# Kernel tuning notes

Hardware: AMD Instinct MI355X
Metric: run time of the kernel (lower is better)

The kernel has to match this reference:

```python
import jax, jax.numpy as jnp
import numpy as np

N = 50000        # nodes
E = 1600000      # edges (avg degree 32)
F = 256          # feature_dim
H = 128          # hidden_dim
ED = 32          # edge_dim
C = 2            # num_classes
GAMMA, ZETA = -0.1, 1.1   # hard-concrete stretch bounds


def setup_inputs() -> dict:
    key = jax.random.key(0)
    ks = jax.random.split(key, 16)
    def p(i, shape, fan):
        return jax.random.normal(ks[i], shape, dtype=jnp.float32) * np.float32(1.0 / np.sqrt(fan))
    return {
        "x": jax.random.normal(ks[0], (N, F), dtype=jnp.float32),
        "edge_index": jax.random.randint(ks[1], (2, E), 0, N, dtype=jnp.int64),
        # edge scorer: Linear(2F -> ED) split into src/dst halves, then Linear(ED -> 1)
        "we_src": p(2, (F, ED), 2 * F),
        "we_dst": p(3, (F, ED), 2 * F),
        "be": jnp.zeros((ED,), jnp.float32),
        "we2": p(4, (ED,), ED),
        "be2": jnp.zeros((), jnp.float32),
        # node transform conv: Linear(F -> H)
        "wc": p(5, (F, H), F),
        "bc": jnp.zeros((H,), jnp.float32),
        # classifier: Linear(H -> H//2), LayerNorm(H//2), spectral_norm(Linear(H//2 -> C))
        "w1": p(6, (H, H // 2), H),
        "b1": jnp.zeros((H // 2,), jnp.float32),
        "ln_g": jnp.ones((H // 2,), jnp.float32),
        "ln_b": jnp.zeros((H // 2,), jnp.float32),
        "w2": p(7, (H // 2, C), H // 2),
        "b2": jnp.zeros((C,), jnp.float32),
    }


def reference(x, edge_index, we_src, we_dst, be, we2, be2, wc, bc,
              w1, b1, ln_g, ln_b, w2, b2):
    src, dst = edge_index[0], edge_index[1]
    n = x.shape[0]

    # --- edge scoring: MLP on (x_src, x_dst); project per-node first, then gather ---
    ps = x @ we_src                       # [N, ED]
    pd = x @ we_dst                       # [N, ED]
    e_h = jax.nn.relu(ps[src] + pd[dst] + be)   # [E, ED]
    logit = e_h @ we2 + be2               # [E]

    # --- hard-concrete L0 gate (deterministic / eval form) ---
    s = jax.nn.sigmoid(logit)
    gate = jnp.clip(s * (ZETA - GAMMA) + GAMMA, 0.0, 1.0)   # [E]

    # --- node transform + edge-gated message passing ---
    h = jax.nn.relu(x @ wc + bc)                            # [N, H]
    agg = jax.ops.segment_sum(gate[:, None] * h[src], dst, num_segments=n)  # [N, H]
    deg = jax.ops.segment_sum(gate, dst, num_segments=n)                    # [N]
    h_out = h + agg / (deg[:, None] + 1e-6)

    # --- edge-weighted attention pooling: attend by gated degree ---
    att = jax.nn.softmax(deg)             # [N]
    g = att @ h_out                       # [H]

    # --- classifier: Linear -> ReLU -> LayerNorm -> spectral_norm(Linear) ---
    z = jax.nn.relu(g @ w1 + b1)          # [H//2]
    mn = z.mean()
    v = ((z - mn) ** 2).mean()
    zn = (z - mn) / jnp.sqrt(v + 1e-5) * ln_g + ln_b
    sigma = jnp.linalg.norm(w2, ord=2)    # spectral norm of weight
    logits = zn @ (w2 / sigma) + b2       # [C]
    return logits
```

## Files before the change

kernel.cpp:

```cpp
#include <hip/hip_runtime.h>
#include <hip/hip_bf16.h>
#include <math.h>

constexpr int F  = 256;
constexpr int ED = 32;
constexpr int H  = 128;
constexpr int NB = 64;
constexpr int SLICE_MAX = 6272;
constexpr int CAP = 26624;
constexpr float CSH = 60.0f;

typedef __attribute__((ext_vector_type(8))) short    short8v;
typedef __attribute__((ext_vector_type(4))) float    float4v;
typedef __attribute__((ext_vector_type(8))) _Float16 half8v;

static __device__ __forceinline__ unsigned short f2bf(float f) {
    unsigned int u = __float_as_uint(f);
    unsigned int r = (u + 0x7FFFu + ((u >> 16) & 1u)) >> 16;
    return (unsigned short)r;
}

__global__ __launch_bounds__(256) void pack_kernel(
    const float* __restrict__ we_src, const float* __restrict__ we_dst,
    const float* __restrict__ wc, unsigned short* __restrict__ Wp,
    float* __restrict__ zbase, int zcount)
{
    if (blockIdx.x >= 24) {
        int zi = (blockIdx.x - 24) * 256 + threadIdx.x;
        if (zi < zcount) zbase[zi] = 0.0f;
        return;
    }
    int id = blockIdx.x * 256 + threadIdx.x;
    if (id >= 12 * 8 * 64) return;
    int lane = id & 63;
    int ks   = (id >> 6) & 7;
    int tile = id >> 9;
    int col  = tile * 16 + (lane & 15);
    int kb   = ks * 32 + (lane >> 4) * 8;

    short8v v;
    #pragma unroll
    for (int j = 0; j < 8; ++j) {
        int k = kb + j;
        float w;
        if (col < 32)       w = we_src[k * ED + col];
        else if (col < 64)  w = we_dst[k * ED + (col - 32)];
        else                w = wc[k * H + (col - 64)];
        v[j] = (short)f2bf(w);
    }
    *(short8v*)(Wp + (size_t)id * 8) = v;
}

__global__ __launch_bounds__(1024) void scatter_kernel(
    const int* __restrict__ ei, int* __restrict__ cursor,
    unsigned* __restrict__ sd, int E, int SL)
{
    __shared__ int lh[NB];
    __shared__ int lbase[NB];
    const int t = threadIdx.x;
    if (t < NB) lh[t] = 0;
    __syncthreads();

    const int e0 = blockIdx.x * 2048 + t;
    unsigned c0 = 0, c1 = 0;
    int k0 = 0, r0 = 0, k1 = 0, r1 = 0;
    const bool v0 = (e0 < E);
    const bool v1 = (e0 + 1024 < E);
    if (v0) {
        int s = ei[e0], d = ei[E + e0];
        int i = (int)((unsigned)s / (unsigned)SL);
        int j = (int)((unsigned)d / (unsigned)SL);
        k0 = i * 8 + j;
        c0 = (unsigned)(s - i * SL) | ((unsigned)(d - j * SL) << 16);
        r0 = atomicAdd(&lh[k0], 1);
    }
    if (v1) {
        int s = ei[e0 + 1024], d = ei[E + e0 + 1024];
        int i = (int)((unsigned)s / (unsigned)SL);
        int j = (int)((unsigned)d / (unsigned)SL);
        k1 = i * 8 + j;
        c1 = (unsigned)(s - i * SL) | ((unsigned)(d - j * SL) << 16);
        r1 = atomicAdd(&lh[k1], 1);
    }
    __syncthreads();
    if (t < NB && lh[t] > 0) lbase[t] = atomicAdd(&cursor[t], lh[t]);
    __syncthreads();
    if (v0) {
        int idx = lbase[k0] + r0;
        if (idx < CAP) sd[(size_t)k0 * CAP + idx] = c0;
    }
    if (v1) {
        int idx = lbase[k1] + r1;
        if (idx < CAP) sd[(size_t)k1 * CAP + idx] = c1;
    }
}

__global__ __launch_bounds__(256) void gemm_kernel(
    const float* __restrict__ x, const unsigned short* __restrict__ Wp,
    const float* __restrict__ bc,
    _Float16* __restrict__ psh, _Float16* __restrict__ pdh,
    _Float16* __restrict__ hh, int M16)
{
    __shared__ __align__(16) unsigned char As[16 * 512];

    const int t    = threadIdx.x;
    const int w    = t >> 6;
    const int lane = t & 63;

    const short8v* WpV = (const short8v*)Wp;
    short8v Bfr[3][8];
    #pragma unroll
    for (int ct = 0; ct < 3; ++ct)
        #pragma unroll
        for (int ks = 0; ks < 8; ++ks)
            Bfr[ct][ks] = WpV[(((w * 3 + ct) * 8 + ks) << 6) + lane];

    const int srow = t >> 4;
    const int sseg = t & 15;
    const int ssw  = (srow & 7) << 4;

    const int arow = lane & 15;
    const int asw  = (arow & 7) << 4;
    const int akb  = (lane >> 4) * 16;

    const int crow0 = (lane >> 4) * 4;
    const int ccol  = lane & 15;

    for (int rt = blockIdx.x; rt < M16; rt += gridDim.x) {
        const int n0 = rt * 16;
        {
            const float4* src = (const float4*)(x + (size_t)(n0 + srow) * F + sseg * 16);
            float4 f0 = src[0], f1 = src[1], f2 = src[2], f3 = src[3];
            short8v lo, hi;
            lo[0] = (short)f2bf(f0.x); lo[1] = (short)f2bf(f0.y);
            lo[2] = (short)f2bf(f0.z); lo[3] = (short)f2bf(f0.w);
            lo[4] = (short)f2bf(f1.x); lo[5] = (short)f2bf(f1.y);
            lo[6] = (short)f2bf(f1.z); lo[7] = (short)f2bf(f1.w);
            hi[0] = (short)f2bf(f2.x); hi[1] = (short)f2bf(f2.y);
            hi[2] = (short)f2bf(f2.z); hi[3] = (short)f2bf(f2.w);
            hi[4] = (short)f2bf(f3.x); hi[5] = (short)f2bf(f3.y);
            hi[6] = (short)f2bf(f3.z); hi[7] = (short)f2bf(f3.w);
            *(short8v*)&As[srow * 512 + ((sseg * 32 +  0) ^ ssw)] = lo;
            *(short8v*)&As[srow * 512 + ((sseg * 32 + 16) ^ ssw)] = hi;
        }
        __syncthreads();

        float4v accs[3];
        #pragma unroll
        for (int ct = 0; ct < 3; ++ct) accs[ct] = (float4v){0.f, 0.f, 0.f, 0.f};

        #pragma unroll
        for (int ks = 0; ks < 8; ++ks) {
            short8v a = *(const short8v*)&As[arow * 512 + ((ks * 64 + akb) ^ asw)];
            accs[0] = __builtin_amdgcn_mfma_f32_16x16x32_bf16(a, Bfr[0][ks], accs[0], 0, 0, 0);
            accs[1] = __builtin_amdgcn_mfma_f32_16x16x32_bf16(a, Bfr[1][ks], accs[1], 0, 0, 0);
            accs[2] = __builtin_amdgcn_mfma_f32_16x16x32_bf16(a, Bfr[2][ks], accs[2], 0, 0, 0);
        }

        #pragma unroll
        for (int ct = 0; ct < 3; ++ct) {
            const int gcol = w * 48 + ct * 16 + ccol;
            #pragma unroll
            for (int r = 0; r < 4; ++r) {
                const int row = n0 + crow0 + r;
                float v = accs[ct][r];
                if (gcol < 32) {
                    psh[(size_t)row * ED + gcol] = (_Float16)v;
                } else if (gcol < 64) {
                    pdh[(size_t)row * ED + (gcol - 32)] = (_Float16)v;
                } else {
                    float b = bc[gcol - 64];
                    hh[(size_t)row * H + (gcol - 64)] = (_Float16)fmaxf(v + b, 0.f);
                }
            }
        }
        __syncthreads();
    }
}

__global__ __launch_bounds__(1024) void edge_gate_kernel(
    const unsigned* __restrict__ sd, const int* __restrict__ cnt,
    const _Float16* __restrict__ psh, const _Float16* __restrict__ pdh,
    const float* __restrict__ be, const float* __restrict__ we2,
    const float* __restrict__ be2,
    _Float16* __restrict__ gateh, float* __restrict__ deg, int N, int SL)
{
    __shared__ float sbe[ED], swe2[ED];
    __shared__ float sdeg[SLICE_MAX];
    const int t = threadIdx.x;
    if (t < ED) { sbe[t] = be[t]; swe2[t] = we2[t]; }
    for (int idx = t; idx < SLICE_MAX; idx += 1024) sdeg[idx] = 0.0f;
    __syncthreads();

    const int j = blockIdx.x & 7;
    const int k = blockIdx.x >> 3;
    const int i = k >> 3;
    const int p = k & 7;
    const int bucket = i * 8 + j;
    const int start = bucket * CAP;
    const int len   = min(cnt[bucket], CAP);
    const int cs = start + (len * p) / 8;
    const int ce = start + (len * (p + 1)) / 8;
    const int ibase = i * SL;
    const int jbase = j * SL;
    const int jlen  = min(SL, N - jbase);
    const int seg = t & 3;

    for (int base = cs; base < ce; base += 256) {
        const int e = base + (t >> 2);
        if (e < ce) {
            const unsigned code = sd[e];
            const int sl = (int)(code & 0xFFFFu);
            const int dl = (int)(code >> 16);
            half8v a  = *(const half8v*)(psh + (size_t)(ibase + sl) * ED + seg * 8);
            half8v bb = *(const half8v*)(pdh + (size_t)(jbase + dl) * ED + seg * 8);
            float part = 0.f;
            #pragma unroll
            for (int jj = 0; jj < 8; ++jj) {
                int kk = seg * 8 + jj;
                part += fmaxf((float)a[jj] + (float)bb[jj] + sbe[kk], 0.f) * swe2[kk];
            }
            part += __shfl_xor(part, 1);
            part += __shfl_xor(part, 2);
            if (seg == 0) {
                float logit = part + be2[0];
                float sg = 1.0f / (1.0f + expf(-logit));
                float gt = fminf(fmaxf(sg * 1.2f - 0.1f, 0.0f), 1.0f);
                gateh[e] = (_Float16)gt;
                if (gt > 0.0f) atomicAdd(&sdeg[dl], gt);
            }
        }
    }
    __syncthreads();

    float* dst = deg + jbase;
    for (int idx = t; idx < jlen; idx += 1024) {
        float v = sdeg[idx];
        if (v != 0.0f) atomicAdd(&dst[idx], v);
    }
}

__global__ __launch_bounds__(1024) void edge_u_kernel(
    const unsigned* __restrict__ sd, const int* __restrict__ cnt,
    const _Float16* __restrict__ gateh, const float* __restrict__ deg,
    float* __restrict__ uraw, int N, int SL)
{
    __shared__ float su[SLICE_MAX];
    const int t = threadIdx.x;
    for (int idx = t; idx < SLICE_MAX; idx += 1024) su[idx] = 0.0f;
    __syncthreads();

    const int j = blockIdx.x & 7;
    const int k = blockIdx.x >> 3;
    const int i = k >> 3;
    const int p = k & 7;
    const int bucket = i * 8 + j;
    const int start = bucket * CAP;
    const int len   = min(cnt[bucket], CAP);
    const int cs = start + (len * p) / 8;
    const int ce = start + (len * (p + 1)) / 8;
    const int ibase = i * SL;
    const int jbase = j * SL;
    const int ilen  = min(SL, N - ibase);

    for (int e = cs + t; e < ce; e += 1024) {
        float gt = (float)gateh[e];
        if (gt != 0.f) {
            unsigned code = sd[e];
            int sl = (int)(code & 0xFFFFu);
            int dl = (int)(code >> 16);
            float dg = deg[jbase + dl];
            float cv = expf(dg - CSH) / (dg + 1e-6f);
            atomicAdd(&su[sl], gt * cv);
        }
    }
    __syncthreads();

    float* dst = uraw + ibase;
    for (int idx = t; idx < ilen; idx += 1024) {
        float v = su[idx];
        if (v != 0.0f) atomicAdd(&dst[idx], v);
    }
}

__global__ __launch_bounds__(256) void pool_kernel(
    const _Float16* __restrict__ hh, const float* __restrict__ deg,
    const float* __restrict__ uraw,
    float* __restrict__ gacc, float* __restrict__ S, int N)
{
    __shared__ float red[16][128];
    const int t = threadIdx.x;
    const int lane = t & 15;
    const int row  = t >> 4;

    float acc[8];
    #pragma unroll
    for (int q = 0; q < 8; ++q) acc[q] = 0.f;
    float sexp = 0.f;

    for (int n = blockIdx.x * 16 + row; n < N; n += gridDim.x * 16) {
        float ex  = expf(deg[n] - CSH);
        float wgt = ex + uraw[n];
        half8v hv = *(const half8v*)(hh + (size_t)n * H + lane * 8);
        #pragma unroll
        for (int q = 0; q < 8; ++q) acc[q] += wgt * (float)hv[q];
        if (lane == 0) sexp += ex;
    }
    sexp += __shfl_xor(sexp, 16);
    sexp += __shfl_xor(sexp, 32);
    if ((t & 63) == 0 && sexp != 0.f) atomicAdd(S, sexp);

    #pragma unroll
    for (int q = 0; q < 8; ++q) red[row][lane * 8 + q] = acc[q];
    __syncthreads();
    if (t < 128) {
        float s = 0.f;
        #pragma unroll
        for (int r = 0; r < 16; ++r) s += red[r][t];
        if (s != 0.f) atomicAdd(&gacc[t], s);
    }
}

__global__ __launch_bounds__(64) void cls_kernel(
    const float* __restrict__ gacc, const float* __restrict__ S,
    const float* __restrict__ w1, const float* __restrict__ b1,
    const float* __restrict__ ln_g, const float* __restrict__ ln_b,
    const float* __restrict__ w2, const float* __restrict__ b2,
    float* __restrict__ out)
{
    __shared__ float gs[H];
    const int t = threadIdx.x;
    const float invS = 1.0f / S[0];
    gs[t]      = gacc[t]      * invS;
    gs[t + 64] = gacc[t + 64] * invS;
    __syncthreads();

    float acc = b1[t];
    #pragma unroll 4
    for (int k = 0; k < H; ++k) acc += gs[k] * w1[k * 64 + t];
    float z = fmaxf(acc, 0.f);

    float sm = z;
    #pragma unroll
    for (int m = 1; m < 64; m <<= 1) sm += __shfl_xor(sm, m);
    float mn = sm * (1.0f / 64.0f);
    float dv = (z - mn) * (z - mn);
    float sv = dv;
    #pragma unroll
    for (int m = 1; m < 64; m <<= 1) sv += __shfl_xor(sv, m);
    float var = sv * (1.0f / 64.0f);

    float zn = (z - mn) * rsqrtf(var + 1e-5f) * ln_g[t] + ln_b[t];

    float w20 = w2[t * 2 + 0];
    float w21 = w2[t * 2 + 1];
    float ga = w20 * w20, gb = w20 * w21, gc = w21 * w21;
    float p0 = zn * w20, p1 = zn * w21;
    #pragma unroll
    for (int m = 1; m < 64; m <<= 1) {
        ga += __shfl_xor(ga, m);
        gb += __shfl_xor(gb, m);
        gc += __shfl_xor(gc, m);
        p0 += __shfl_xor(p0, m);
        p1 += __shfl_xor(p1, m);
    }
    if (t == 0) {
        float tr = ga + gc;
        float df = ga - gc;
        float eig = 0.5f * (tr + sqrtf(df * df + 4.0f * gb * gb));
        float sigma = sqrtf(eig);
        out[0] = p0 / sigma + b2[0];
        out[1] = p1 / sigma + b2[1];
    }
}

extern "C" void kernel_launch(void* const* d_in, const int* in_sizes, int n_in,
                              void* d_out, int out_size, void* d_ws, size_t ws_size,
                              hipStream_t stream) {
    const float* x      = (const float*)d_in[0];
    const int*   ei     = (const int*)  d_in[1];
    const float* we_src = (const float*)d_in[2];
    const float* we_dst = (const float*)d_in[3];
    const float* be     = (const float*)d_in[4];
    const float* we2    = (const float*)d_in[5];
    const float* be2    = (const float*)d_in[6];
    const float* wc     = (const float*)d_in[7];
    const float* bc     = (const float*)d_in[8];
    const float* w1     = (const float*)d_in[9];
    const float* b1     = (const float*)d_in[10];
    const float* ln_g   = (const float*)d_in[11];
    const float* ln_b   = (const float*)d_in[12];
    const float* w2     = (const float*)d_in[13];
    const float* b2     = (const float*)d_in[14];

    const int N = in_sizes[0] / F;
    const int E = in_sizes[1] / 2;
    const int M16 = N / 16;
    const int SL = (N + 7) / 8;

    float* ws = (float*)d_ws;
    size_t off = 0;
    float* zbase = ws;
    float* deg  = ws + off; off += (size_t)N;
    float* uraw = ws + off; off += (size_t)N;
    float* gacc = ws + off; off += 128;
    float* S    = ws + off; off += 1;
    int*   cursor = (int*)(ws + off); off += NB;
    const int zcount = (int)off;
    off = (off + 15) & ~(size_t)15;
    unsigned short* Wp = (unsigned short*)(ws + off); off += (12 * 8 * 64 * 8) / 2;
    off = (off + 15) & ~(size_t)15;
    _Float16* psh = (_Float16*)(ws + off); off += (size_t)N * ED / 2;
    _Float16* pdh = (_Float16*)(ws + off); off += (size_t)N * ED / 2;
    _Float16* hh  = (_Float16*)(ws + off); off += (size_t)N * H / 2;
    _Float16* gateh = (_Float16*)(ws + off); off += (size_t)NB * CAP / 2;
    unsigned* sd = (unsigned*)(ws + off); off += (size_t)NB * CAP;

    const int zblocks = (zcount + 255) / 256;
    pack_kernel<<<24 + zblocks, 256, 0, stream>>>(we_src, we_dst, wc, Wp, zbase, zcount);
    scatter_kernel<<<(E + 2047) / 2048, 1024, 0, stream>>>(ei, cursor, sd, E, SL);
    gemm_kernel<<<1024, 256, 0, stream>>>(x, Wp, bc, psh, pdh, hh, M16);
    edge_gate_kernel<<<512, 1024, 0, stream>>>(sd, cursor, psh, pdh, be, we2, be2,
                                               gateh, deg, N, SL);
    edge_u_kernel<<<512, 1024, 0, stream>>>(sd, cursor, gateh, deg, uraw, N, SL);
    pool_kernel<<<512, 256, 0, stream>>>(hh, deg, uraw, gacc, S, N);
    cls_kernel<<<1, 64, 0, stream>>>(gacc, S, w1, b1, ln_g, ln_b, w2, b2,
                                     (float*)d_out);
}
```

Baseline: 147.4 us.

## Fuse edge bucketing scatter into GEMM launch as extra heterogeneous blocks

Merges the edge scatter/bucketing kernel into the node GEMM kernel by appending scatter blocks to the same grid, selected by block index. Scatter blocks now use 256 threads processing 8 edges each instead of 1024 threads processing 2. This removes one launch and the serialization between two independent stages, letting the memory-bound scatter overlap with the GEMM. The risk is that GEMM blocks' register and LDS footprint now applies to scatter blocks, lowering their occupancy, and block scheduling order may delay overlap.

```diff
diff --git a/kernel.cpp b/kernel.cpp
--- a/kernel.cpp
+++ b/kernel.cpp
@@ -51,59 +51,54 @@
     *(short8v*)(Wp + (size_t)id * 8) = v;
 }
 
-__global__ __launch_bounds__(1024) void scatter_kernel(
-    const int* __restrict__ ei, int* __restrict__ cursor,
-    unsigned* __restrict__ sd, int E, int SL)
-{
-    __shared__ int lh[NB];
-    __shared__ int lbase[NB];
-    const int t = threadIdx.x;
-    if (t < NB) lh[t] = 0;
-    __syncthreads();
-
-    const int e0 = blockIdx.x * 2048 + t;
-    unsigned c0 = 0, c1 = 0;
-    int k0 = 0, r0 = 0, k1 = 0, r1 = 0;
-    const bool v0 = (e0 < E);
-    const bool v1 = (e0 + 1024 < E);
-    if (v0) {
-        int s = ei[e0], d = ei[E + e0];
-        int i = (int)((unsigned)s / (unsigned)SL);
-        int j = (int)((unsigned)d / (unsigned)SL);
-        k0 = i * 8 + j;
-        c0 = (unsigned)(s - i * SL) | ((unsigned)(d - j * SL) << 16);
-        r0 = atomicAdd(&lh[k0], 1);
-    }
-    if (v1) {
-        int s = ei[e0 + 1024], d = ei[E + e0 + 1024];
-        int i = (int)((unsigned)s / (unsigned)SL);
-        int j = (int)((unsigned)d / (unsigned)SL);
-        k1 = i * 8 + j;
-        c1 = (unsigned)(s - i * SL) | ((unsigned)(d - j * SL) << 16);
-        r1 = atomicAdd(&lh[k1], 1);
-    }
-    __syncthreads();
-    if (t < NB && lh[t] > 0) lbase[t] = atomicAdd(&cursor[t], lh[t]);
-    __syncthreads();
-    if (v0) {
-        int idx = lbase[k0] + r0;
-        if (idx < CAP) sd[(size_t)k0 * CAP + idx] = c0;
-    }
-    if (v1) {
-        int idx = lbase[k1] + r1;
-        if (idx < CAP) sd[(size_t)k1 * CAP + idx] = c1;
-    }
-}
-
-__global__ __launch_bounds__(256) void gemm_kernel(
+__global__ __launch_bounds__(256) void gemm_scatter_kernel(
     const float* __restrict__ x, const unsigned short* __restrict__ Wp,
     const float* __restrict__ bc,
     _Float16* __restrict__ psh, _Float16* __restrict__ pdh,
-    _Float16* __restrict__ hh, int M16)
+    _Float16* __restrict__ hh, int M16,
+    const int* __restrict__ ei, int* __restrict__ cursor,
+    unsigned* __restrict__ sd, int E, int SL, int gemmBlocks)
 {
     __shared__ __align__(16) unsigned char As[16 * 512];
-
-    const int t    = threadIdx.x;
+    __shared__ int lh[NB];
+    __shared__ int lbase[NB];
+
+    const int t = threadIdx.x;
+
+    if (blockIdx.x >= gemmBlocks) {
+        const int sblk = blockIdx.x - gemmBlocks;
+        if (t < NB) lh[t] = 0;
+        __syncthreads();
+
+        unsigned code[8];
+        int key[8], r[8];
+        bool val[8];
+        #pragma unroll
+        for (int q = 0; q < 8; ++q) {
+            const int e = sblk * 2048 + q * 256 + t;
+            val[q] = (e < E);
+            if (val[q]) {
+                int s = ei[e], d = ei[E + e];
+                int i = (int)((unsigned)s / (unsigned)SL);
+                int j = (int)((unsigned)d / (unsigned)SL);
+                key[q] = i * 8 + j;
+                code[q] = (unsigned)(s - i * SL) | ((unsigned)(d - j * SL) << 16);
+                r[q] = atomicAdd(&lh[key[q]], 1);
+            }
+        }
+        __syncthreads();
+        if (t < NB && lh[t] > 0) lbase[t] = atomicAdd(&cursor[t], lh[t]);
+        __syncthreads();
+        #pragma unroll
+        for (int q = 0; q < 8; ++q) {
+            if (val[q]) {
+                int idx = lbase[key[q]] + r[q];
+                if (idx < CAP) sd[(size_t)key[q] * CAP + idx] = code[q];
+            }
+        }
+        return;
+    }
+
     const int w    = t >> 6;
     const int lane = t & 63;
 
@@ -126,7 +121,7 @@
     const int crow0 = (lane >> 4) * 4;
     const int ccol  = lane & 15;
 
-    for (int rt = blockIdx.x; rt < M16; rt += gridDim.x) {
+    for (int rt = blockIdx.x; rt < M16; rt += gemmBlocks) {
         const int n0 = rt * 16;
         {
             const float4* src = (const float4*)(x + (size_t)(n0 + srow) * F + sseg * 16);
@@ -417,9 +412,12 @@
     unsigned* sd = (unsigned*)(ws + off); off += (size_t)NB * CAP;
 
     const int zblocks = (zcount + 255) / 256;
+    const int gemmBlocks = 1024;
+    const int scatBlocks = (E + 2047) / 2048;
+
     pack_kernel<<<24 + zblocks, 256, 0, stream>>>(we_src, we_dst, wc, Wp, zbase, zcount);
-    scatter_kernel<<<(E + 2047) / 2048, 1024, 0, stream>>>(ei, cursor, sd, E, SL);
-    gemm_kernel<<<1024, 256, 0, stream>>>(x, Wp, bc, psh, pdh, hh, M16);
+    gemm_scatter_kernel<<<gemmBlocks + scatBlocks, 256, 0, stream>>>(
+        x, Wp, bc, psh, pdh, hh, M16, ei, cursor, sd, E, SL, gemmBlocks);
     edge_gate_kernel<<<512, 1024, 0, stream>>>(sd, cursor, psh, pdh, be, we2, be2,
                                                gateh, deg, N, SL);
     edge_u_kernel<<<512, 1024, 0, stream>>>(sd, cursor, gateh, deg, uraw, N, SL);
```

New measurement: 143.7 us. -2.5%, faster.
